# Kernel tuning notes

Hardware: AMD Instinct MI355X
Metric: run time of the kernel (lower is better)

The kernel has to match this reference:

```python
import jax, jax.numpy as jnp
import numpy as np

NUM_HEADS = 8
MASK_NEG = -1e30


def setup_inputs() -> dict:
    key = jax.random.key(0)
    k1, k2, k3 = jax.random.split(key, 3)
    B, S, D = 8, 2048, 128
    queries = jax.random.normal(k1, (B, S, D), dtype=jnp.float32)
    mask = jnp.ones((B, S), dtype=jnp.float32)
    # kernel_size=1 Conv1D with no bias == dense matmul over last dim
    W_q = jax.random.normal(k2, (D, D), dtype=jnp.float32) * (D ** -0.5)
    W_mem = jax.random.normal(k3, (D, 2 * D), dtype=jnp.float32) * (D ** -0.5)
    return {"queries": queries, "mask": mask, "W_q": W_q, "W_mem": W_mem}


def _split_heads(x, h):
    # [B, S, D] -> [B, h, S, D/h]
    B, S, D = x.shape
    return x.reshape(B, S, h, D // h).transpose(0, 2, 1, 3)


def reference(queries, mask, W_q, W_mem):
    B, S, D = queries.shape
    h = NUM_HEADS
    scale = (D // h) ** -0.5
    memory = jnp.einsum('bsd,de->bse', queries, W_mem)   # [B,S,2D]
    query = jnp.einsum('bsd,de->bse', queries, W_q)      # [B,S,D]
    K, V = jnp.split(memory, 2, axis=2)
    Q = _split_heads(query, h) * scale                   # [B,h,S,dh]
    K = _split_heads(K, h)
    V = _split_heads(V, h)
    logits = jnp.einsum('bhqd,bhkd->bhqk', Q, K)         # [B,h,S,S]
    m = mask.reshape(B, 1, 1, S)
    logits = logits + (1.0 - m) * MASK_NEG
    weights = jax.nn.softmax(logits, axis=-1)
    # dropout is identity at inference (training=None)
    x = jnp.einsum('bhqk,bhkd->bhqd', weights, V)        # [B,h,S,dh]
    return x.transpose(0, 2, 1, 3).reshape(B, S, D)
```

## Files before the change

### kernel.cpp

```cpp
#include <hip/hip_runtime.h>
#include <hip/hip_bf16.h>
#include <stdint.h>

#define B_    8
#define S_    2048
#define D_    128
#define H_    8
#define DH_   16
#define BH_   64
#define E_    384
#define NT_   (S_ / 32)

typedef __attribute__((ext_vector_type(4)))  short short4v;
typedef __attribute__((ext_vector_type(8)))  short short8;
typedef __attribute__((ext_vector_type(4)))  float f32x4;
typedef __attribute__((ext_vector_type(16))) float f32x16;

__device__ inline unsigned short f2b(float f) {
    union { __bf16 h; unsigned short u; } t;
    t.h = (__bf16)f;
    return t.u;
}
__device__ inline float b2f(unsigned short u) {
    union { unsigned u; float f; } x; x.u = ((unsigned)u) << 16; return x.f;
}
__device__ inline int dperm(int d) {
    return (d & 3) | ((d & 8) >> 1) | ((d & 4) << 1);
}

__device__ inline void gload_lds16(const void* g, void* l) {
    __builtin_amdgcn_global_load_lds(
        (const __attribute__((address_space(1))) unsigned int*)g,
        (__attribute__((address_space(3))) unsigned int*)l, 16, 0, 0);
}

#define EXPB 16250.7346f

__global__ void wtrans_kernel(const float* __restrict__ Wq,
                              const float* __restrict__ Wmem,
                              unsigned short* __restrict__ wt) {
    int e = blockIdx.x, k = threadIdx.x;
    float v = (e < 128) ? Wq[k * 128 + e] : Wmem[k * 256 + (e - 128)];
    wt[e * 128 + k] = f2b(v);
}

__global__ __launch_bounds__(512) void proj_kernel(
        const float* __restrict__ X, const float* __restrict__ mask,
        const unsigned short* __restrict__ wt,
        unsigned short* __restrict__ Qb, unsigned short* __restrict__ KVf) {
    __shared__ unsigned short Xs[64][136];
    __shared__ unsigned short Vs[64][136];
    __shared__ __align__(16) unsigned short Qls[64][136];
    __shared__ __align__(16) unsigned short Kls[8][2][64][8];
    __shared__ float Ms[64];
    const int tid = threadIdx.x;
    const int b = blockIdx.x & 7, st = blockIdx.x >> 3;
    const int s0 = st * 64;
    const float* Xp = X + ((size_t)b * S_ + s0) * D_;

    for (int i = tid; i < 64 * D_ / 4; i += 512) {
        f32x4 v = __builtin_nontemporal_load((const f32x4*)Xp + i);
        int row = i >> 5, c4 = (i & 31) * 4;
        Xs[row][c4 + 0] = f2b(v[0]); Xs[row][c4 + 1] = f2b(v[1]);
        Xs[row][c4 + 2] = f2b(v[2]); Xs[row][c4 + 3] = f2b(v[3]);
    }
    if (tid < 64) Ms[tid] = mask[(size_t)b * S_ + s0 + tid];
    __syncthreads();

    const int wid = tid >> 6, lane = tid & 63;
    const int lr = lane & 15, lg = lane >> 4;
    const float qscale = 0.25f * 1.44269504088896f;

    for (int ci = 0; ci < 3; ++ci) {
        const int ct = wid + ci * 8;
        const int e0 = ct * 16;
        short4v bfr[8];
        #pragma unroll
        for (int kk = 0; kk < 8; ++kk)
            bfr[kk] = *(const short4v*)&wt[(e0 + lr) * 128 + kk * 16 + lg * 4];
        for (int rt = 0; rt < 4; ++rt) {
            f32x4 acc; acc[0] = acc[1] = acc[2] = acc[3] = 0.f;
            #pragma unroll
            for (int kk = 0; kk < 8; ++kk) {
                short4v a = *(const short4v*)&Xs[rt * 16 + lr][kk * 16 + lg * 4];
                acc = __builtin_amdgcn_mfma_f32_16x16x16bf16_1k(a, bfr[kk], acc, 0, 0, 0);
            }
            const int e = e0 + lr;
            #pragma unroll
            for (int r = 0; r < 4; ++r) {
                const int sl = rt * 16 + lg * 4 + r;
                const float v = acc[r];
                if (e < 128) {
                    int hh = e >> 4, d = dperm(e & 15);
                    Qls[sl][hh * 16 + d] = f2b(v * qscale);
                } else if (e < 256) {
                    int ek = e - 128, hh = ek >> 4, d = dperm(ek & 15);
                    int t = sl >> 5, qq = sl & 31;
                    int l = qq + 32 * (d >> 3), jj = d & 7;
                    Kls[hh][t][l][jj] = f2b(v);
                } else {
                    Vs[sl][e - 256] = f2b(v);
                }
            }
        }
    }
    __syncthreads();

    for (int c = tid; c < 1024; c += 512) {
        const int hh = c >> 7, sl = (c >> 1) & 63, half = c & 1;
        *(short8*)&Qb[(((size_t)b * H_ + hh) * S_ + s0 + sl) * DH_ + half * 8] =
            *(const short8*)&Qls[sl][hh * 16 + half * 8];
    }
    for (int c = tid; c < 1024; c += 512) {
        const int hh = c >> 7, t = (c >> 6) & 1, lc = c & 63;
        *(short8*)&KVf[((size_t)(b * H_ + hh) * NT_ + st * 2 + t) * 1536 + lc * 8] =
            *(const short8*)&Kls[hh][t][lc][0];
    }

    for (int j = tid; j < H_ * 2 * 2 * 64; j += 512) {
        const int l = j & 63, f = (j >> 6) & 1, t = (j >> 7) & 1, hh = j >> 8;
        const int q = l & 31, h = l >> 5;
        const int vrow = (q < 16) ? q : 16;
        const int T = st * 2 + t;
        unsigned short* dst =
            KVf + ((size_t)(b * H_ + hh) * NT_ + T) * 1536 + (1 + f) * 512 + l * 8;
        union { unsigned short us[8]; short8 v; } o;
        #pragma unroll
        for (int e = 0; e < 8; ++e) {
            const int p = f * 16 + 8 * h + e;
            const int sl = (p & 16) | dperm(p & 15);
            const int srow = t * 32 + sl;
            const float mk = Ms[srow];
            o.us[e] = f2b((vrow == 16) ? mk : b2f(Vs[srow][hh * 16 + vrow]) * mk);
        }
        *(short8*)dst = o.v;
    }
}

__global__ __launch_bounds__(512, 4) void attn_kernel(
        const unsigned short* __restrict__ Qb, const unsigned short* __restrict__ KVf,
        float* __restrict__ out) {
    const int tid = threadIdx.x;
    const int wid = tid >> 6, lane = tid & 63;
    const int q = lane & 31, h = lane >> 5;
    const int p = blockIdx.x;
    const int bh = (p & 7) * 8 + ((p >> 3) & 7);
    const int qs = p >> 6;
    const int q0 = qs * 256 + wid * 32;

    __shared__ unsigned short buf[2][8][3][64][8];

    const unsigned short* kv = KVf + (size_t)bh * NT_ * 1536 + (size_t)lane * 8;

    const short8 qf = *(const short8*)&Qb[((size_t)bh * S_ + q0 + q) * DH_ + 8 * h];

    f32x16 accA, accB, z;
    #pragma unroll
    for (int i = 0; i < 16; ++i) { accA[i] = 0.f; accB[i] = 0.f; z[i] = 0.f; }

#define STAGE(C_)                                                              \
    {                                                                          \
        const int tt_ = (C_) * 4 + (wid & 3) + ((wid >> 2) * 32);              \
        const unsigned short* g_ = kv + (size_t)tt_ * 1536;                    \
        unsigned short* d_ = &buf[(C_) & 1][wid][0][0][0];                     \
        gload_lds16(g_,        d_);                                            \
        gload_lds16(g_ + 512,  d_ + 512);                                      \
        gload_lds16(g_ + 1024, d_ + 1024);                                     \
    }

#define TILE_BODY(ACC_, BI_, T_)                                               \
    {                                                                          \
        const short8 kf  = *(const short8*)&buf[BI_][T_][0][lane][0];          \
        const short8 va0 = *(const short8*)&buf[BI_][T_][1][lane][0];          \
        const short8 va1 = *(const short8*)&buf[BI_][T_][2][lane][0];          \
        __builtin_amdgcn_s_setprio(1);                                         \
        f32x16 s0 = __builtin_amdgcn_mfma_f32_32x32x16_bf16(kf, qf, z, 0, 0, 0); \
        __builtin_amdgcn_s_setprio(0);                                         \
        union { unsigned u[4]; short8 v; } b0, b1;                             \
        _Pragma("unroll")                                                      \
        for (int i = 0; i < 4; ++i) {                                          \
            const int l0 = (int)__builtin_fmaf(s0[2 * i],     128.f, EXPB);    \
            const int h0 = (int)__builtin_fmaf(s0[2 * i + 1], 128.f, EXPB);    \
            b0.u[i] = (unsigned)l0 | ((unsigned)h0 << 16);                     \
            const int l1 = (int)__builtin_fmaf(s0[8 + 2 * i],     128.f, EXPB);\
            const int h1 = (int)__builtin_fmaf(s0[8 + 2 * i + 1], 128.f, EXPB);\
            b1.u[i] = (unsigned)l1 | ((unsigned)h1 << 16);                     \
        }                                                                      \
        __builtin_amdgcn_s_setprio(1);                                         \
        ACC_ = __builtin_amdgcn_mfma_f32_32x32x16_bf16(va0, b0.v, ACC_, 0, 0, 0); \
        ACC_ = __builtin_amdgcn_mfma_f32_32x32x16_bf16(va1, b1.v, ACC_, 0, 0, 0); \
        __builtin_amdgcn_s_setprio(0);                                         \
    }

    STAGE(0);

    for (int c = 0; c < 8; ++c) {
        asm volatile("s_waitcnt lgkmcnt(0) vmcnt(0)" ::: "memory");
        __builtin_amdgcn_sched_barrier(0);
        __builtin_amdgcn_s_barrier();
        __builtin_amdgcn_sched_barrier(0);
        if (c < 7) STAGE(c + 1);
        const int bi = c & 1;
        #pragma unroll
        for (int i = 0; i < 4; ++i) {
            TILE_BODY(accA, bi, i);
            TILE_BODY(accB, bi, 4 + i);
        }
    }
#undef STAGE
#undef TILE_BODY

    const int b = bh >> 3, head = bh & 7;
    float* obase = out + ((size_t)b * S_ + q0 + q) * D_ + head * DH_ + 4 * h;
    float o[16];
    #pragma unroll
    for (int i = 0; i < 16; ++i) o[i] = accA[i] + accB[i];
    const float r = 1.0f / o[8];
    *(float4*)obase       = make_float4(o[0] * r, o[1] * r, o[2] * r, o[3] * r);
    *(float4*)(obase + 8) = make_float4(o[4] * r, o[5] * r, o[6] * r, o[7] * r);
}

extern "C" void kernel_launch(void* const* d_in, const int* in_sizes, int n_in,
                              void* d_out, int out_size, void* d_ws, size_t ws_size,
                              hipStream_t stream) {
    const float* X    = (const float*)d_in[0];
    const float* mask = (const float*)d_in[1];
    const float* Wq   = (const float*)d_in[2];
    const float* Wmem = (const float*)d_in[3];
    float* out = (float*)d_out;

    unsigned short* Qb  = (unsigned short*)d_ws;
    unsigned short* KVf = Qb + (size_t)BH_ * S_ * DH_;
    unsigned short* wt  = KVf + (size_t)BH_ * NT_ * 1536;

    wtrans_kernel<<<E_, 128, 0, stream>>>(Wq, Wmem, wt);
    proj_kernel<<<B_ * S_ / 64, 512, 0, stream>>>(X, mask, wt, Qb, KVf);
    attn_kernel<<<BH_ * 8, 512, 0, stream>>>(Qb, KVf, out);
}
```

Measured before the change: 55.69 us.

## Software-pipeline QK MFMA one tile ahead of exp and PV in attention loop

Restructures the attention inner loop so the QK^T MFMAs for the next tile pair are issued before the exp-conversion and PV MFMAs of the current pair. A prologue primes the first scores, and an epilogue drains the last. The intent is to hide MFMA latency and the VALU exp work behind independent matrix ops. It also drops the s_setprio hints and raises register pressure from the extra live score and V fragments, which could reduce occupancy.

```diff
diff --git a/kernel.cpp b/kernel.cpp
--- a/kernel.cpp
+++ b/kernel.cpp
@@ -158,6 +158,9 @@
     #pragma unroll
     for (int i = 0; i < 16; ++i) { accA[i] = 0.f; accB[i] = 0.f; z[i] = 0.f; }
 
+    f32x16 sA, sB;
+    short8 pA0, pA1, pB0, pB1;
+
 #define STAGE(C_)                                                              \
     {                                                                          \
         const int tt_ = (C_) * 4 + (wid & 3) + ((wid >> 2) * 32);              \
@@ -168,47 +171,79 @@
         gload_lds16(g_ + 1024, d_ + 1024);                                     \
     }
 
-#define TILE_BODY(ACC_, BI_, T_)                                               \
-    {                                                                          \
-        const short8 kf  = *(const short8*)&buf[BI_][T_][0][lane][0];          \
-        const short8 va0 = *(const short8*)&buf[BI_][T_][1][lane][0];          \
-        const short8 va1 = *(const short8*)&buf[BI_][T_][2][lane][0];          \
-        __builtin_amdgcn_s_setprio(1);                                         \
-        f32x16 s0 = __builtin_amdgcn_mfma_f32_32x32x16_bf16(kf, qf, z, 0, 0, 0); \
-        __builtin_amdgcn_s_setprio(0);                                         \
+#define FENCE_BAR()                                                            \
+    asm volatile("s_waitcnt lgkmcnt(0) vmcnt(0)" ::: "memory");                \
+    __builtin_amdgcn_sched_barrier(0);                                         \
+    __builtin_amdgcn_s_barrier();                                              \
+    __builtin_amdgcn_sched_barrier(0);
+
+#define EXP_PV(ACC_, S_, V0_, V1_)                                             \
+    {                                                                          \
         union { unsigned u[4]; short8 v; } b0, b1;                             \
         _Pragma("unroll")                                                      \
         for (int i = 0; i < 4; ++i) {                                          \
-            const int l0 = (int)__builtin_fmaf(s0[2 * i],     128.f, EXPB);    \
-            const int h0 = (int)__builtin_fmaf(s0[2 * i + 1], 128.f, EXPB);    \
+            const int l0 = (int)__builtin_fmaf(S_[2 * i],     128.f, EXPB);    \
+            const int h0 = (int)__builtin_fmaf(S_[2 * i + 1], 128.f, EXPB);    \
             b0.u[i] = (unsigned)l0 | ((unsigned)h0 << 16);                     \
-            const int l1 = (int)__builtin_fmaf(s0[8 + 2 * i],     128.f, EXPB);\
-            const int h1 = (int)__builtin_fmaf(s0[8 + 2 * i + 1], 128.f, EXPB);\
+            const int l1 = (int)__builtin_fmaf(S_[8 + 2 * i],     128.f, EXPB);\
+            const int h1 = (int)__builtin_fmaf(S_[8 + 2 * i + 1], 128.f, EXPB);\
             b1.u[i] = (unsigned)l1 | ((unsigned)h1 << 16);                     \
         }                                                                      \
-        __builtin_amdgcn_s_setprio(1);                                         \
-        ACC_ = __builtin_amdgcn_mfma_f32_32x32x16_bf16(va0, b0.v, ACC_, 0, 0, 0); \
-        ACC_ = __builtin_amdgcn_mfma_f32_32x32x16_bf16(va1, b1.v, ACC_, 0, 0, 0); \
-        __builtin_amdgcn_s_setprio(0);                                         \
+        ACC_ = __builtin_amdgcn_mfma_f32_32x32x16_bf16(V0_, b0.v, ACC_, 0, 0, 0); \
+        ACC_ = __builtin_amdgcn_mfma_f32_32x32x16_bf16(V1_, b1.v, ACC_, 0, 0, 0); \
+    }
+
+#define PAIR_STEP(BI_, I_)                                                     \
+    {                                                                          \
+        const short8 kfA = *(const short8*)&buf[BI_][I_][0][lane][0];          \
+        const short8 nA0 = *(const short8*)&buf[BI_][I_][1][lane][0];          \
+        const short8 nA1 = *(const short8*)&buf[BI_][I_][2][lane][0];          \
+        const short8 kfB = *(const short8*)&buf[BI_][4 + I_][0][lane][0];      \
+        const short8 nB0 = *(const short8*)&buf[BI_][4 + I_][1][lane][0];      \
+        const short8 nB1 = *(const short8*)&buf[BI_][4 + I_][2][lane][0];      \
+        f32x16 nsA = __builtin_amdgcn_mfma_f32_32x32x16_bf16(kfA, qf, z, 0, 0, 0); \
+        f32x16 nsB = __builtin_amdgcn_mfma_f32_32x32x16_bf16(kfB, qf, z, 0, 0, 0); \
+        EXP_PV(accA, sA, pA0, pA1);                                            \
+        EXP_PV(accB, sB, pB0, pB1);                                            \
+        sA = nsA; sB = nsB;                                                    \
+        pA0 = nA0; pA1 = nA1; pB0 = nB0; pB1 = nB1;                            \
+    }
+
+#define PRIME(BI_, I_)                                                         \
+    {                                                                          \
+        const short8 kfA = *(const short8*)&buf[BI_][I_][0][lane][0];          \
+        pA0 = *(const short8*)&buf[BI_][I_][1][lane][0];                       \
+        pA1 = *(const short8*)&buf[BI_][I_][2][lane][0];                       \
+        const short8 kfB = *(const short8*)&buf[BI_][4 + I_][0][lane][0];      \
+        pB0 = *(const short8*)&buf[BI_][4 + I_][1][lane][0];                   \
+        pB1 = *(const short8*)&buf[BI_][4 + I_][2][lane][0];                   \
+        sA = __builtin_amdgcn_mfma_f32_32x32x16_bf16(kfA, qf, z, 0, 0, 0);     \
+        sB = __builtin_amdgcn_mfma_f32_32x32x16_bf16(kfB, qf, z, 0, 0, 0);     \
     }
 
     STAGE(0);
+    FENCE_BAR();
+    STAGE(1);
+    PRIME(0, 0);
 
     for (int c = 0; c < 8; ++c) {
-        asm volatile("s_waitcnt lgkmcnt(0) vmcnt(0)" ::: "memory");
-        __builtin_amdgcn_sched_barrier(0);
-        __builtin_amdgcn_s_barrier();
-        __builtin_amdgcn_sched_barrier(0);
-        if (c < 7) STAGE(c + 1);
-        const int bi = c & 1;
+        if (c > 0) {
+            FENCE_BAR();
+            if (c < 7) STAGE(c + 1);
+        }
         #pragma unroll
         for (int i = 0; i < 4; ++i) {
-            TILE_BODY(accA, bi, i);
-            TILE_BODY(accB, bi, 4 + i);
-        }
-    }
+            if (c == 0 && i == 0) continue;
+            PAIR_STEP(c & 1, i);
+        }
+    }
+    EXP_PV(accA, sA, pA0, pA1);
+    EXP_PV(accB, sB, pB0, pB1);
 #undef STAGE
-#undef TILE_BODY
+#undef FENCE_BAR
+#undef EXP_PV
+#undef PAIR_STEP
+#undef PRIME
 
     const int b = bh >> 3, head = bh & 7;
     float* obase = out + ((size_t)b * S_ + q0 + q) * D_ + head * DH_ + 4 * h;
```

After: 54.58 us. 1.02x faster.

## Give each wave private double-buffered K/V slabs and software-pipeline QK with PV

Applied to the files above, without the earlier changes.

The attention kernel moves from 512-thread blocks covering 256 queries to 256-thread blocks covering 128 queries, doubling the grid. Each wave now streams its own K/V tiles into a private LDS slab with asynchronous loads, which removes the block-wide barrier. The loop is software-pipelined so the QK MFMA for the next tile is issued while the exp and PV MFMAs of the previous tile run, using vmcnt waits instead of full drains. Every wave now loads all 64 tiles itself rather than sharing a staged buffer across eight waves, so global and L2 traffic per query rises.

```diff
diff --git a/kernel.cpp b/kernel.cpp
--- a/kernel.cpp
+++ b/kernel.cpp
@@ -137,7 +137,7 @@
     }
 }
 
-__global__ __launch_bounds__(512, 4) void attn_kernel(
+__global__ __launch_bounds__(256, 3) void attn_kernel(
         const unsigned short* __restrict__ Qb, const unsigned short* __restrict__ KVf,
         float* __restrict__ out) {
     const int tid = threadIdx.x;
@@ -145,10 +145,10 @@
     const int q = lane & 31, h = lane >> 5;
     const int p = blockIdx.x;
     const int bh = (p & 7) * 8 + ((p >> 3) & 7);
-    const int qs = p >> 6;
-    const int q0 = qs * 256 + wid * 32;
-
-    __shared__ unsigned short buf[2][8][3][64][8];
+    const int qt = p >> 6;
+    const int q0 = qt * 128 + wid * 32;
+
+    __shared__ unsigned short slab[4][2][2][3][64][8];
 
     const unsigned short* kv = KVf + (size_t)bh * NT_ * 1536 + (size_t)lane * 8;
 
@@ -158,57 +158,97 @@
     #pragma unroll
     for (int i = 0; i < 16; ++i) { accA[i] = 0.f; accB[i] = 0.f; z[i] = 0.f; }
 
-#define STAGE(C_)                                                              \
+    f32x16 sA, sB;
+    short8 pA0, pA1, pB0, pB1;
+
+#define STAGE_PAIR(X_, SL_)                                                    \
     {                                                                          \
-        const int tt_ = (C_) * 4 + (wid & 3) + ((wid >> 2) * 32);              \
-        const unsigned short* g_ = kv + (size_t)tt_ * 1536;                    \
-        unsigned short* d_ = &buf[(C_) & 1][wid][0][0][0];                     \
-        gload_lds16(g_,        d_);                                            \
-        gload_lds16(g_ + 512,  d_ + 512);                                      \
-        gload_lds16(g_ + 1024, d_ + 1024);                                     \
-    }
-
-#define TILE_BODY(ACC_, BI_, T_)                                               \
+        const unsigned short* gA_ = kv + (size_t)(X_) * 1536;                  \
+        const unsigned short* gB_ = kv + (size_t)(32 + (X_)) * 1536;           \
+        unsigned short* dA_ = &slab[wid][SL_][0][0][0][0];                     \
+        unsigned short* dB_ = &slab[wid][SL_][1][0][0][0];                     \
+        gload_lds16(gA_,        dA_);                                          \
+        gload_lds16(gA_ + 512,  dA_ + 512);                                    \
+        gload_lds16(gA_ + 1024, dA_ + 1024);                                   \
+        gload_lds16(gB_,        dB_);                                          \
+        gload_lds16(gB_ + 512,  dB_ + 512);                                    \
+        gload_lds16(gB_ + 1024, dB_ + 1024);                                   \
+    }
+
+#define EXP_PV(ACC_, S_, V0_, V1_)                                             \
     {                                                                          \
-        const short8 kf  = *(const short8*)&buf[BI_][T_][0][lane][0];          \
-        const short8 va0 = *(const short8*)&buf[BI_][T_][1][lane][0];          \
-        const short8 va1 = *(const short8*)&buf[BI_][T_][2][lane][0];          \
-        __builtin_amdgcn_s_setprio(1);                                         \
-        f32x16 s0 = __builtin_amdgcn_mfma_f32_32x32x16_bf16(kf, qf, z, 0, 0, 0); \
-        __builtin_amdgcn_s_setprio(0);                                         \
         union { unsigned u[4]; short8 v; } b0, b1;                             \
         _Pragma("unroll")                                                      \
         for (int i = 0; i < 4; ++i) {                                          \
-            const int l0 = (int)__builtin_fmaf(s0[2 * i],     128.f, EXPB);    \
-            const int h0 = (int)__builtin_fmaf(s0[2 * i + 1], 128.f, EXPB);    \
+            const int l0 = (int)__builtin_fmaf(S_[2 * i],     128.f, EXPB);    \
+            const int h0 = (int)__builtin_fmaf(S_[2 * i + 1], 128.f, EXPB);    \
             b0.u[i] = (unsigned)l0 | ((unsigned)h0 << 16);                     \
-            const int l1 = (int)__builtin_fmaf(s0[8 + 2 * i],     128.f, EXPB);\
-            const int h1 = (int)__builtin_fmaf(s0[8 + 2 * i + 1], 128.f, EXPB);\
+            const int l1 = (int)__builtin_fmaf(S_[8 + 2 * i],     128.f, EXPB);\
+            const int h1 = (int)__builtin_fmaf(S_[8 + 2 * i + 1], 128.f, EXPB);\
             b1.u[i] = (unsigned)l1 | ((unsigned)h1 << 16);                     \
         }                                                                      \
-        __builtin_amdgcn_s_setprio(1);                                         \
-        ACC_ = __builtin_amdgcn_mfma_f32_32x32x16_bf16(va0, b0.v, ACC_, 0, 0, 0); \
-        ACC_ = __builtin_amdgcn_mfma_f32_32x32x16_bf16(va1, b1.v, ACC_, 0, 0, 0); \
-        __builtin_amdgcn_s_setprio(0);                                         \
-    }
-
-    STAGE(0);
-
-    for (int c = 0; c < 8; ++c) {
-        asm volatile("s_waitcnt lgkmcnt(0) vmcnt(0)" ::: "memory");
+        ACC_ = __builtin_amdgcn_mfma_f32_32x32x16_bf16(V0_, b0.v, ACC_, 0, 0, 0); \
+        ACC_ = __builtin_amdgcn_mfma_f32_32x32x16_bf16(V1_, b1.v, ACC_, 0, 0, 0); \
+    }
+
+    STAGE_PAIR(0, 0);
+    STAGE_PAIR(1, 1);
+    asm volatile("s_waitcnt vmcnt(6)" ::: "memory");
+    __builtin_amdgcn_sched_barrier(0);
+    {
+        const short8 kfA = *(const short8*)&slab[wid][0][0][0][lane][0];
+        pA0 = *(const short8*)&slab[wid][0][0][1][lane][0];
+        pA1 = *(const short8*)&slab[wid][0][0][2][lane][0];
+        const short8 kfB = *(const short8*)&slab[wid][0][1][0][lane][0];
+        pB0 = *(const short8*)&slab[wid][0][1][1][lane][0];
+        pB1 = *(const short8*)&slab[wid][0][1][2][lane][0];
+        sA = __builtin_amdgcn_mfma_f32_32x32x16_bf16(kfA, qf, z, 0, 0, 0);
+        sB = __builtin_amdgcn_mfma_f32_32x32x16_bf16(kfB, qf, z, 0, 0, 0);
+    }
+    asm volatile("s_waitcnt lgkmcnt(0)" ::: "memory");
+    __builtin_amdgcn_sched_barrier(0);
+    STAGE_PAIR(2, 0);
+
+    #pragma unroll 2
+    for (int t = 1; t <= 30; ++t) {
+        const int sl = t & 1;
+        asm volatile("s_waitcnt vmcnt(6)" ::: "memory");
         __builtin_amdgcn_sched_barrier(0);
-        __builtin_amdgcn_s_barrier();
+        const short8 kfA = *(const short8*)&slab[wid][sl][0][0][lane][0];
+        const short8 nA0 = *(const short8*)&slab[wid][sl][0][1][lane][0];
+        const short8 nA1 = *(const short8*)&slab[wid][sl][0][2][lane][0];
+        const short8 kfB = *(const short8*)&slab[wid][sl][1][0][lane][0];
+        const short8 nB0 = *(const short8*)&slab[wid][sl][1][1][lane][0];
+        const short8 nB1 = *(const short8*)&slab[wid][sl][1][2][lane][0];
+        EXP_PV(accA, sA, pA0, pA1);
+        EXP_PV(accB, sB, pB0, pB1);
+        sA = __builtin_amdgcn_mfma_f32_32x32x16_bf16(kfA, qf, z, 0, 0, 0);
+        sB = __builtin_amdgcn_mfma_f32_32x32x16_bf16(kfB, qf, z, 0, 0, 0);
+        pA0 = nA0; pA1 = nA1; pB0 = nB0; pB1 = nB1;
+        asm volatile("s_waitcnt lgkmcnt(0)" ::: "memory");
         __builtin_amdgcn_sched_barrier(0);
-        if (c < 7) STAGE(c + 1);
-        const int bi = c & 1;
-        #pragma unroll
-        for (int i = 0; i < 4; ++i) {
-            TILE_BODY(accA, bi, i);
-            TILE_BODY(accB, bi, 4 + i);
-        }
-    }
-#undef STAGE
-#undef TILE_BODY
+        if (t < 30) STAGE_PAIR(t + 2, sl);
+    }
+
+    asm volatile("s_waitcnt vmcnt(0)" ::: "memory");
+    __builtin_amdgcn_sched_barrier(0);
+    {
+        const short8 kfA = *(const short8*)&slab[wid][1][0][0][lane][0];
+        const short8 nA0 = *(const short8*)&slab[wid][1][0][1][lane][0];
+        const short8 nA1 = *(const short8*)&slab[wid][1][0][2][lane][0];
+        const short8 kfB = *(const short8*)&slab[wid][1][1][0][lane][0];
+        const short8 nB0 = *(const short8*)&slab[wid][1][1][1][lane][0];
+        const short8 nB1 = *(const short8*)&slab[wid][1][1][2][lane][0];
+        EXP_PV(accA, sA, pA0, pA1);
+        EXP_PV(accB, sB, pB0, pB1);
+        sA = __builtin_amdgcn_mfma_f32_32x32x16_bf16(kfA, qf, z, 0, 0, 0);
+        sB = __builtin_amdgcn_mfma_f32_32x32x16_bf16(kfB, qf, z, 0, 0, 0);
+        pA0 = nA0; pA1 = nA1; pB0 = nB0; pB1 = nB1;
+    }
+    EXP_PV(accA, sA, pA0, pA1);
+    EXP_PV(accB, sB, pB0, pB1);
+#undef STAGE_PAIR
+#undef EXP_PV
 
     const int b = bh >> 3, head = bh & 7;
     float* obase = out + ((size_t)b * S_ + q0 + q) * D_ + head * DH_ + 4 * h;
@@ -235,5 +275,5 @@
 
     wtrans_kernel<<<E_, 128, 0, stream>>>(Wq, Wmem, wt);
     proj_kernel<<<B_ * S_ / 64, 512, 0, stream>>>(X, mask, wt, Qb, KVf);
-    attn_kernel<<<BH_ * 8, 512, 0, stream>>>(Qb, KVf, out);
-}
+    attn_kernel<<<BH_ * (S_ / 128), 256, 0, stream>>>(Qb, KVf, out);
+}
```

After: 60.99 us. +9.5%, slower.
